# Optimization experiments

Hardware: AMD Instinct MI355X
Metric: run time of the kernel (lower is better)

Reference implementation:

```python
import jax, jax.numpy as jnp
import numpy as np

NUM_NODES = 512
INPUT_DIM = 64
HID_DIM = 64
K_DIFF = 2          # max_diffusion_step
N_LAYERS = 2
N_SUPPORTS = 1      # filter_type='laplacian'
NUM_MATS = N_SUPPORTS * K_DIFF + 1
CONCAT = INPUT_DIM + HID_DIM  # == HID_DIM + HID_DIM since input_dim == hid_dim


def setup_inputs() -> dict:
    key = jax.random.key(0)
    ks = jax.random.split(key, 8)
    T, B = 48, 32
    inputs = jax.random.normal(ks[0], (T, B, NUM_NODES * INPUT_DIM), dtype=jnp.float32)
    h0 = jnp.zeros((N_LAYERS, B, NUM_NODES * HID_DIM), dtype=jnp.float32)
    supports = jax.random.uniform(ks[1], (N_SUPPORTS, NUM_NODES, NUM_NODES), dtype=jnp.float32) / NUM_NODES
    s = 0.05
    W_gate = jax.random.normal(ks[2], (N_LAYERS, NUM_MATS * CONCAT, 2 * HID_DIM), dtype=jnp.float32) * s
    b_gate = jnp.ones((N_LAYERS, 2 * HID_DIM), dtype=jnp.float32)  # bias_start=1.0
    W_c = jax.random.normal(ks[3], (N_LAYERS, NUM_MATS * CONCAT, HID_DIM), dtype=jnp.float32) * s
    b_c = jnp.zeros((N_LAYERS, HID_DIM), dtype=jnp.float32)
    return {"inputs": inputs, "initial_hidden_state": h0, "supports": supports,
            "W_gate": W_gate, "b_gate": b_gate, "W_c": W_c, "b_c": b_c}


def _gconv(supports, x_flat, h_flat, W, b, out_dim):
    # x_flat: (B, N*d_in), h_flat: (B, N*hid)
    B = x_flat.shape[0]
    xh = jnp.concatenate([x_flat.reshape(B, NUM_NODES, -1),
                          h_flat.reshape(B, NUM_NODES, -1)], axis=-1)  # (B,N,c)
    mats = [xh]
    for i in range(N_SUPPORTS):
        S = supports[i]
        t0, t1 = xh, jnp.einsum('nm,bmc->bnc', S, xh)
        mats.append(t1)
        for _ in range(2, K_DIFF + 1):  # Chebyshev recurrence: x_k = 2 S x_{k-1} - x_{k-2}
            t2 = 2.0 * jnp.einsum('nm,bmc->bnc', S, t1) - t0
            mats.append(t2)
            t0, t1 = t1, t2
    feat = jnp.concatenate(mats, axis=-1)            # (B, N, NUM_MATS*c)
    out = jnp.einsum('bnf,fo->bno', feat, W) + b      # (B, N, out_dim)
    return out


def _dcgru_cell(supports, x, h, Wg, bg, Wc, bc):
    B = x.shape[0]
    gates = jax.nn.sigmoid(_gconv(supports, x, h, Wg, bg, 2 * HID_DIM))  # (B,N,2h)
    r, u = jnp.split(gates, 2, axis=-1)
    rh = (r * h.reshape(B, NUM_NODES, HID_DIM)).reshape(B, NUM_NODES * HID_DIM)
    c = jnp.tanh(_gconv(supports, x, rh, Wc, bc, HID_DIM))               # (B,N,h)
    h3 = h.reshape(B, NUM_NODES, HID_DIM)
    new_h = u * h3 + (1.0 - u) * c
    return new_h.reshape(B, NUM_NODES * HID_DIM)


def reference(inputs, initial_hidden_state, supports, W_gate, b_gate, W_c, b_c):
    current = inputs  # (T, B, N*d)
    final_hidden = []
    for l in range(N_LAYERS):
        def step(h, x, l=l):
            h2 = _dcgru_cell(supports, x, h, W_gate[l], b_gate[l], W_c[l], b_c[l])
            return h2, h2
        hT, outs = jax.lax.scan(step, initial_hidden_state[l], current)
        final_hidden.append(hT)
        current = outs
    return jnp.stack(final_hidden, axis=0), current
```

## Files before the change

kernel.cpp:

```cpp
#include <hip/hip_runtime.h>
#include <math.h>

typedef __bf16 bf16_t;
typedef bf16_t bf16x8 __attribute__((ext_vector_type(8)));
typedef bf16_t bf16x4 __attribute__((ext_vector_type(4)));
typedef float  f32x4  __attribute__((ext_vector_type(4)));
typedef unsigned long long u64_t;

#define NB 32
#define NN 512
#define NH 64
#define NF 384
#define TSTEPS 48

static __device__ __forceinline__ f32x4 mfma16(bf16x8 a, bf16x8 b, f32x4 c){
  return __builtin_amdgcn_mfma_f32_16x16x32_bf16(a, b, c, 0, 0, 0);
}
static __device__ __forceinline__ void gload16(char* lds, const char* g){
  __builtin_amdgcn_global_load_lds((const __attribute__((address_space(1))) void*)g,
                                   (__attribute__((address_space(3))) void*)lds, 16, 0, 0);
}
static __device__ __forceinline__ unsigned pack2(float a, float b){
  bf16_t x = (bf16_t)a, y = (bf16_t)b;
  unsigned short ux = __builtin_bit_cast(unsigned short, x);
  unsigned short uy = __builtin_bit_cast(unsigned short, y);
  return (unsigned)ux | ((unsigned)uy << 16);
}

__global__ __launch_bounds__(256) void k_s2f(const float* __restrict__ S,
                                             float* __restrict__ S2f){
  int idx = blockIdx.x * 256 + threadIdx.x;
  int n = idx >> 9, m = idx & 511;
  float acc = 0.f;
  #pragma unroll 8
  for (int k = 0; k < 512; ++k) acc += S[n * 512 + k] * S[k * 512 + m];
  S2f[idx] = acc;
}

__global__ __launch_bounds__(256) void k_prepS(const float* __restrict__ S,
                                               const float* __restrict__ S2f,
                                               char* __restrict__ dst){
  int id = blockIdx.x * 256 + threadIdx.x;
  int r = id >> 9, k = id & 511;
  float v = (r < 512) ? S[r * 512 + k] : S2f[(r - 512) * 512 + k];
  int rt = r >> 5, rr = r & 31, kt = k >> 6, kk = k & 63;
  size_t off = ((size_t)(rt * 8 + kt)) * 4096 + (size_t)(((rr * 128 + 2 * kk)) ^ ((rr & 7) << 4));
  *(bf16_t*)(dst + off) = (bf16_t)v;
}

__global__ __launch_bounds__(256) void k_prepW(const float* __restrict__ W,
                                               char* __restrict__ dst, int OD){
  int i = blockIdx.x * 256 + threadIdx.x;
  int total = 2 * NF * OD;
  if (i >= total) return;
  int l = i / (NF * OD), rem = i - l * (NF * OD);
  int o = rem / NF, f = rem - o * NF;
  const float* Wl = W + (size_t)l * NF * OD;
  float v;
  if (f < 128)      v = Wl[f * OD + o] - Wl[(256 + f) * OD + o];
  else if (f < 256) v = Wl[f * OD + o];
  else              v = 2.f * Wl[f * OD + o];
  int kt = f >> 6, kk = f & 63;
  size_t off = (size_t)l * (6 * OD * 128) + (size_t)kt * (OD * 128)
             + (size_t)(((o * 128 + 2 * kk)) ^ ((o & 7) << 4));
  *(bf16_t*)(dst + off) = (bf16_t)v;
}

__global__ __launch_bounds__(256) void k_hinit(const float* __restrict__ h0,
                                               float* __restrict__ hNf,
                                               bf16_t* __restrict__ hN){
  size_t i = ((size_t)blockIdx.x * 256 + threadIdx.x) * 8;
  f32x4 a = *(const f32x4*)&h0[i], b = *(const f32x4*)&h0[i + 4];
  *(f32x4*)&hNf[i] = a; *(f32x4*)&hNf[i + 4] = b;
  bf16x8 v;
  #pragma unroll
  for (int q = 0; q < 4; ++q){ v[q] = (bf16_t)a[q]; v[q + 4] = (bf16_t)b[q]; }
  *(bf16x8*)&hN[i] = v;
}

__global__ __launch_bounds__(512, 4) void k_gate(
    const float* __restrict__ inputs, const float* __restrict__ curp, int p,
    const bf16_t* __restrict__ hN, const char* __restrict__ SP,
    const char* __restrict__ WgP, const float* __restrict__ bga,
    bf16_t* __restrict__ rhN, float* __restrict__ uN, bf16_t* __restrict__ Dx)
{
  const int l = blockIdx.y;
  const int t = p - l;
  if (t < 0 || t >= TSTEPS) return;

  __shared__ char smem[81920];
  char* const A0 = smem;            char* const A1 = smem + 16384;
  char* const B0 = smem + 32768;    char* const B1 = smem + 49152;
  char* const FT = smem;
  char* const W0 = smem + 49152;
  char* const W1 = smem + 65536;
  char* const RL = smem + 49152;
  char* const UL = smem + 57344;

  const int L = blockIdx.x;
  const int b  = (L & 7) + ((L >> 6) << 3);
  const int bx = (L >> 3) & 7;
  const int n0 = bx * 64;
  const int tid = threadIdx.x, lane = tid & 63, w = tid >> 6;
  const int fr = lane & 15, ko = (lane >> 4) * 8, ro = (lane >> 4) * 4;
  const int pp = tid >> 4, q4 = tid & 15;
  const int wr = w >> 2, wc = w & 3;
  const int wn = w & 1, wo = w >> 1;

  const float* xall = l ? curp : inputs;
  const float*  xs = xall + ((size_t)t * NB + b) * NN * NH;
  const bf16_t* hbg = hN + ((size_t)(l * NB + b)) * NN * NH;
  const char* const WgPl = WgP + (size_t)l * 98304;
  const float* const bg = bga + l * 128;
  bf16_t* const rh_l = rhN + (size_t)l * NB * NN * NH;
  float*  const u_l  = uN  + (size_t)l * NB * NN * NH;
  bf16_t* const Dx_l = Dx  + (size_t)l * NB * NN * 128;

  f32x4 acc[4][2] = {};
  f32x4 rx0[2], rx1[2]; u64_t rh0[2], rh1[2];
  char* const Abuf[2] = { A0, A1 };
  char* const Bbuf[2] = { B0, B1 };

  auto ldB = [&](int kt, int s){
    int m = kt * 64 + 2 * pp;
    const float* xr = xs + (size_t)m * NH + q4 * 4;
    rx0[s] = *(const f32x4*)xr; rx1[s] = *(const f32x4*)(xr + NH);
    const bf16_t* hr = hbg + (size_t)m * NH + q4 * 4;
    rh0[s] = *(const u64_t*)hr; rh1[s] = *(const u64_t*)(hr + NH);
  };
  auto stB = [&](int s, char* Bb){
    int mby = 4 * pp;
    #pragma unroll
    for (int i = 0; i < 4; ++i){
      int c = q4 * 4 + i;
      *(unsigned*)(Bb + ((c * 128 + mby) ^ (((c >> 2) & 7) << 4))) = pack2(rx0[s][i], rx1[s][i]);
      int c2 = c + 64;
      unsigned uh = (unsigned)((rh0[s] >> (16 * i)) & 0xffffULL)
                  | ((unsigned)((rh1[s] >> (16 * i)) & 0xffffULL) << 16);
      *(unsigned*)(Bb + ((c2 * 128 + mby) ^ (((c2 >> 2) & 7) << 4))) = uh;
    }
  };
  auto gloadA = [&](int kt, char* Ab){
    #pragma unroll
    for (int i = 0; i < 2; ++i){
      int c = w * 2 + i;
      int ti = c >> 2;
      int rt = (ti < 2) ? (bx * 2 + ti) : (16 + bx * 2 + (ti - 2));
      gload16(Ab + c * 1024,
              SP + ((size_t)(rt * 8 + kt)) * 4096 + (c & 3) * 1024 + lane * 16);
    }
  };
  auto gloadW = [&](int j, char* Wb){
    const char* src = WgPl + (size_t)j * 16384 + (w * 64 + lane) * 16;
    gload16(Wb + w * 1024, src);
    gload16(Wb + 8192 + w * 1024, src + 8192);
  };
  auto dmm = [&](const char* Ab, const char* Bb){
    #pragma unroll
    for (int kh = 0; kh < 2; ++kh){
      int kb = 2 * (kh * 32 + ko);
      bf16x8 af[4], bf_[2];
      #pragma unroll
      for (int fm = 0; fm < 4; ++fm){
        int r = wr * 64 + fm * 16 + fr;
        af[fm] = *(const bf16x8*)(Ab + (r >> 5) * 4096 + ((((r & 31) * 128 + kb)) ^ ((r & 7) << 4)));
      }
      #pragma unroll
      for (int fc = 0; fc < 2; ++fc){
        int c = wc * 32 + fc * 16 + fr;
        bf_[fc] = *(const bf16x8*)(Bb + ((c * 128 + kb) ^ (((c >> 2) & 7) << 4)));
      }
      #pragma unroll
      for (int fm = 0; fm < 4; ++fm)
        #pragma unroll
        for (int fc = 0; fc < 2; ++fc)
          acc[fm][fc] = mfma16(af[fm], bf_[fc], acc[fm][fc]);
    }
  };

  gloadA(0, A0);
  ldB(0, 0); stB(0, B0);
  ldB(1, 1);
  __syncthreads();

  #pragma unroll
  for (int kt = 0; kt < 8; ++kt){
    if (kt < 7){
      gloadA(kt + 1, Abuf[(kt + 1) & 1]);
      stB((kt + 1) & 1, Bbuf[(kt + 1) & 1]);
    }
    dmm(Abuf[kt & 1], Bbuf[kt & 1]);
    __syncthreads();
    if (kt < 6) ldB(kt + 2, (kt + 2) & 1);
  }

  gloadW(0, W0); gloadW(1, W1);

  #pragma unroll
  for (int s = 0; s < 2; ++s){
    int i = tid + s * 512;
    int row = i >> 4, c8 = (i & 15) * 8;
    char* fdst = FT + (((row * 768 + 2 * c8)) ^ ((row & 7) << 4));
    if (c8 < 64){
      const float* xr = xs + (size_t)(n0 + row) * NH + c8;
      f32x4 a = *(const f32x4*)xr, bq = *(const f32x4*)(xr + 4);
      bf16x8 v;
      #pragma unroll
      for (int q = 0; q < 4; ++q){ v[q] = (bf16_t)a[q]; v[q + 4] = (bf16_t)bq[q]; }
      *(bf16x8*)fdst = v;
    } else {
      *(bf16x8*)fdst = *(const bf16x8*)(hbg + (size_t)(n0 + row) * NH + (c8 - 64));
    }
  }
  #pragma unroll
  for (int fm = 0; fm < 4; ++fm)
    #pragma unroll
    for (int fc = 0; fc < 2; ++fc)
      #pragma unroll
      for (int q = 0; q < 4; ++q){
        int dr = wr * 64 + fm * 16 + ro + q;
        int nn = dr & 63;
        int col = ((dr < 64) ? 128 : 256) + wc * 32 + fc * 16 + fr;
        *(bf16_t*)(FT + (((nn * 768 + 2 * col)) ^ ((nn & 7) << 4))) = (bf16_t)acc[fm][fc][q];
      }
  __syncthreads();

  #pragma unroll
  for (int s = 0; s < 2; ++s){
    int i = tid + s * 512;
    int row = i >> 4, d8 = (i & 15) * 8;
    int col = (d8 < 64) ? 128 + d8 : 256 + (d8 - 64);
    bf16x8 v = *(const bf16x8*)(FT + (((row * 768 + 2 * col)) ^ ((row & 7) << 4)));
    *(bf16x8*)&Dx_l[((size_t)b * NN + n0 + row) * 128 + d8] = v;
  }

  f32x4 gd[2][2] = {};
  #pragma unroll
  for (int j = 0; j < 6; ++j){
    const char* Wb = (j & 1) ? W1 : W0;
    #pragma unroll
    for (int kh = 0; kh < 2; ++kh){
      int kbf = 2 * (j * 64 + kh * 32 + ko);
      int kbw = 2 * (kh * 32 + ko);
      bf16x8 af[2];
      #pragma unroll
      for (int fm = 0; fm < 2; ++fm){
        int r = wn * 32 + fm * 16 + fr;
        af[fm] = *(const bf16x8*)(FT + ((r * 768 + kbf) ^ ((r & 7) << 4)));
      }
      #pragma unroll
      for (int fo = 0; fo < 2; ++fo){
        int orow = wo * 32 + fo * 16 + fr;
        bf16x8 bw = *(const bf16x8*)(Wb + ((orow * 128 + kbw) ^ ((orow & 7) << 4)));
        #pragma unroll
        for (int fm = 0; fm < 2; ++fm)
          gd[fm][fo] = mfma16(af[fm], bw, gd[fm][fo]);
      }
    }
    if (j != 4) __syncthreads();
    if (j < 4) gloadW(j + 2, (j & 1) ? W1 : W0);
  }

  #pragma unroll
  for (int fm = 0; fm < 2; ++fm)
    #pragma unroll
    for (int fo = 0; fo < 2; ++fo){
      int o = wo * 32 + fo * 16 + fr;
      float bias = bg[o];
      #pragma unroll
      for (int q = 0; q < 4; ++q){
        int nn = wn * 32 + fm * 16 + ro + q;
        float g = 1.f / (1.f + __expf(-(gd[fm][fo][q] + bias)));
        if (o < 64){
          float hv = (float)*(const bf16_t*)(FT + (((nn * 768 + 2 * (64 + o))) ^ ((nn & 7) << 4)));
          *(bf16_t*)(RL + ((nn * 128 + 2 * o) ^ ((nn & 7) << 4))) = (bf16_t)(g * hv);
        } else {
          *(float*)(UL + ((nn * 256 + 4 * (o - 64)) ^ ((nn & 7) << 5))) = g;
        }
      }
    }
  __syncthreads();
  {
    int row = tid >> 3, o8 = (tid & 7) * 8;
    bf16x8 v = *(const bf16x8*)(RL + ((row * 128 + 2 * o8) ^ ((row & 7) << 4)));
    *(bf16x8*)&rh_l[((size_t)b * NN + n0 + row) * NH + o8] = v;
    int base = (row * 256 + 4 * o8) ^ ((row & 7) << 5);
    f32x4 u0 = *(const f32x4*)(UL + base);
    f32x4 u1 = *(const f32x4*)(UL + base + 16);
    size_t gi = ((size_t)b * NN + n0 + row) * NH + o8;
    *(f32x4*)&u_l[gi] = u0; *(f32x4*)&u_l[gi + 4] = u1;
  }
}

__global__ __launch_bounds__(512, 4) void k_cand(
    const float* __restrict__ inputs, int p,
    const bf16_t* __restrict__ rhN, const bf16_t* __restrict__ Dx,
    const char* __restrict__ SP, const char* __restrict__ WcP,
    const float* __restrict__ bca, const float* __restrict__ uN,
    float* __restrict__ hNf, bf16_t* __restrict__ hN,
    float* __restrict__ outp)
{
  const int l = blockIdx.y;
  const int t = p - l;
  if (t < 0 || t >= TSTEPS) return;

  __shared__ char smem[81920];
  char* const A0 = smem;            char* const A1 = smem + 16384;
  char* const B0 = smem + 32768;    char* const B1 = smem + 40960;
  char* const FT = smem;
  char* const W0 = smem + 49152;    char* const W1 = smem + 65536;
  char* const CL = smem + 49152;

  const int L = blockIdx.x;
  const int b  = (L & 7) + ((L >> 6) << 3);
  const int bx = (L >> 3) & 7;
  const int n0 = bx * 64;
  const int tid = threadIdx.x, lane = tid & 63, w = tid >> 6;
  const int fr = lane & 15, ko = (lane >> 4) * 8, ro = (lane >> 4) * 4;
  const int pp = tid >> 4, q4 = tid & 15;
  const int wr = w >> 2, wc = w & 3;
  const int wn = w & 1, wo = w >> 1;

  float* const cur = outp + (size_t)2 * NB * NN * NH;
  const float* xall = l ? cur : inputs;
  const float*  xs = xall + ((size_t)t * NB + b) * NN * NH;
  const bf16_t* rbg = rhN + ((size_t)(l * NB + b)) * NN * NH;
  const char* const WcPl = WcP + (size_t)l * 49152;
  const float* const bc = bca + l * 64;
  const bf16_t* const Dx_l = Dx + (size_t)l * NB * NN * 128;
  const float* const u_l = uN + (size_t)l * NB * NN * NH;
  float*  const hNf_l = hNf + (size_t)l * NB * NN * NH;
  bf16_t* const hN_l  = hN  + (size_t)l * NB * NN * NH;
  float* const fin = outp + (size_t)l * NB * NN * NH;

  f32x4 ca[4] = {};
  u64_t rh0[2], rh1[2];
  char* const Abuf[2] = { A0, A1 };
  char* const Bbuf[2] = { B0, B1 };

  auto ldB = [&](int kt, int s){
    int m = kt * 64 + 2 * pp;
    const bf16_t* rr = rbg + (size_t)m * NH + q4 * 4;
    rh0[s] = *(const u64_t*)rr; rh1[s] = *(const u64_t*)(rr + NH);
  };
  auto stB = [&](int s, char* Bb){
    int mby = 4 * pp;
    #pragma unroll
    for (int i = 0; i < 4; ++i){
      int c = q4 * 4 + i;
      unsigned u = (unsigned)((rh0[s] >> (16 * i)) & 0xffffULL)
                 | ((unsigned)((rh1[s] >> (16 * i)) & 0xffffULL) << 16);
      *(unsigned*)(Bb + ((c * 128 + mby) ^ (((c >> 2) & 7) << 4))) = u;
    }
  };
  auto gloadA = [&](int kt, char* Ab){
    #pragma unroll
    for (int i = 0; i < 2; ++i){
      int c = w * 2 + i;
      int ti = c >> 2;
      int rt = (ti < 2) ? (bx * 2 + ti) : (16 + bx * 2 + (ti - 2));
      gload16(Ab + c * 1024,
              SP + ((size_t)(rt * 8 + kt)) * 4096 + (c & 3) * 1024 + lane * 16);
    }
  };
  auto gloadW2 = [&](int j, char* Wb){
    const char* src = WcPl + (size_t)(2 * j) * 8192 + (w * 64 + lane) * 16;
    gload16(Wb + w * 1024, src);
    gload16(Wb + 8192 + w * 1024, src + 8192);
  };
  auto cmm = [&](const char* Ab, const char* Bb){
    #pragma unroll
    for (int kh = 0; kh < 2; ++kh){
      int kb = 2 * (kh * 32 + ko);
      int c = wc * 16 + fr;
      bf16x8 bf_ = *(const bf16x8*)(Bb + ((c * 128 + kb) ^ (((c >> 2) & 7) << 4)));
      #pragma unroll
      for (int fm = 0; fm < 4; ++fm){
        int r = wr * 64 + fm * 16 + fr;
        bf16x8 af = *(const bf16x8*)(Ab + (r >> 5) * 4096 + ((((r & 31) * 128 + kb)) ^ ((r & 7) << 4)));
        ca[fm] = mfma16(af, bf_, ca[fm]);
      }
    }
  };

  gloadA(0, A0);
  gloadW2(0, W0); gloadW2(1, W1);
  ldB(0, 0); stB(0, B0);
  ldB(1, 1);
  __syncthreads();

  #pragma unroll
  for (int kt = 0; kt < 8; ++kt){
    if (kt < 7){
      gloadA(kt + 1, Abuf[(kt + 1) & 1]);
      stB((kt + 1) & 1, Bbuf[(kt + 1) & 1]);
    }
    cmm(Abuf[kt & 1], Bbuf[kt & 1]);
    __syncthreads();
    if (kt < 6) ldB(kt + 2, (kt + 2) & 1);
  }

  #pragma unroll
  for (int s = 0; s < 2; ++s){
    int i = tid + s * 512;
    int row = i >> 4, c8 = (i & 15) * 8;
    char* fdst = FT + (((row * 768 + 2 * c8)) ^ ((row & 7) << 4));
    if (c8 < 64){
      const float* xr = xs + (size_t)(n0 + row) * NH + c8;
      f32x4 a = *(const f32x4*)xr, bq = *(const f32x4*)(xr + 4);
      bf16x8 v;
      #pragma unroll
      for (int q = 0; q < 4; ++q){ v[q] = (bf16_t)a[q]; v[q + 4] = (bf16_t)bq[q]; }
      *(bf16x8*)fdst = v;
    } else {
      *(bf16x8*)fdst = *(const bf16x8*)(rbg + (size_t)(n0 + row) * NH + (c8 - 64));
    }
    int col = (c8 < 64) ? 128 + c8 : 256 + (c8 - 64);
    bf16x8 dv = *(const bf16x8*)&Dx_l[((size_t)b * NN + n0 + row) * 128 + c8];
    *(bf16x8*)(FT + (((row * 768 + 2 * col)) ^ ((row & 7) << 4))) = dv;
  }
  #pragma unroll
  for (int fm = 0; fm < 4; ++fm)
    #pragma unroll
    for (int q = 0; q < 4; ++q){
      int dr = wr * 64 + fm * 16 + ro + q;
      int nn = dr & 63;
      int col = ((dr < 64) ? 192 : 320) + wc * 16 + fr;
      *(bf16_t*)(FT + (((nn * 768 + 2 * col)) ^ ((nn & 7) << 4))) = (bf16_t)ca[fm][q];
    }
  __syncthreads();

  f32x4 cd[2] = {};
  #pragma unroll
  for (int j = 0; j < 3; ++j){
    const char* Wb = (j & 1) ? W1 : W0;
    #pragma unroll
    for (int kh = 0; kh < 4; ++kh){
      int kbf = 2 * (j * 128 + kh * 32 + ko);
      int sub = (kh >= 2) ? 8192 : 0;
      int kbw = 2 * ((kh & 1) * 32 + ko);
      int orow = wo * 16 + fr;
      bf16x8 bw = *(const bf16x8*)(Wb + sub + ((orow * 128 + kbw) ^ ((orow & 7) << 4)));
      #pragma unroll
      for (int fm = 0; fm < 2; ++fm){
        int r = wn * 32 + fm * 16 + fr;
        bf16x8 af = *(const bf16x8*)(FT + ((r * 768 + kbf) ^ ((r & 7) << 4)));
        cd[fm] = mfma16(af, bw, cd[fm]);
      }
    }
    __syncthreads();
    if (j == 0) gloadW2(2, W0);
  }

  #pragma unroll
  for (int fm = 0; fm < 2; ++fm){
    int o = wo * 16 + fr;
    float bias = bc[o];
    #pragma unroll
    for (int q = 0; q < 4; ++q){
      int nn = wn * 32 + fm * 16 + ro + q;
      float e = __expf(2.f * (cd[fm][q] + bias));
      *(float*)(CL + ((nn * 256 + 4 * o) ^ ((nn & 7) << 5))) = (e - 1.f) / (e + 1.f);
    }
  }
  __syncthreads();
  {
    int row = tid >> 3, o8 = (tid & 7) * 8;
    int base = (row * 256 + 4 * o8) ^ ((row & 7) << 5);
    f32x4 c0 = *(const f32x4*)(CL + base);
    f32x4 c1 = *(const f32x4*)(CL + base + 16);
    size_t gi = ((size_t)b * NN + n0 + row) * NH + o8;
    f32x4 u0 = *(const f32x4*)&u_l[gi], u1 = *(const f32x4*)&u_l[gi + 4];
    f32x4 h0v = *(const f32x4*)&hNf_l[gi], h1v = *(const f32x4*)&hNf_l[gi + 4];
    f32x4 n0v, n1v;
    #pragma unroll
    for (int q = 0; q < 4; ++q){
      n0v[q] = u0[q] * h0v[q] + (1.f - u0[q]) * c0[q];
      n1v[q] = u1[q] * h1v[q] + (1.f - u1[q]) * c1[q];
    }
    *(f32x4*)&hNf_l[gi] = n0v; *(f32x4*)&hNf_l[gi + 4] = n1v;
    bf16x8 hb;
    #pragma unroll
    for (int q = 0; q < 4; ++q){ hb[q] = (bf16_t)n0v[q]; hb[q + 4] = (bf16_t)n1v[q]; }
    *(bf16x8*)&hN_l[gi] = hb;
    float* cr = cur + (size_t)t * NB * NN * NH + gi;
    *(f32x4*)cr = n0v; *(f32x4*)(cr + 4) = n1v;
    if (t == TSTEPS - 1){
      *(f32x4*)&fin[gi] = n0v; *(f32x4*)&fin[gi + 4] = n1v;
    }
  }
}

extern "C" void kernel_launch(void* const* d_in, const int* in_sizes, int n_in,
                              void* d_out, int out_size, void* d_ws, size_t ws_size,
                              hipStream_t stream){
  const float* inputs = (const float*)d_in[0];
  const float* h0     = (const float*)d_in[1];
  const float* S      = (const float*)d_in[2];
  const float* W_gate = (const float*)d_in[3];
  const float* b_gate = (const float*)d_in[4];
  const float* W_c    = (const float*)d_in[5];
  const float* b_c    = (const float*)d_in[6];
  float* out = (float*)d_out;
  char* ws = (char*)d_ws;

  char*   SP  =          ws + 0;
  char*   WgP =          ws + 1048576;
  char*   WcP =          ws + 1245184;
  float*  hNf = (float*) (ws + 1343488);
  bf16_t* hN  = (bf16_t*)(ws + 9732096);
  bf16_t* rhN = (bf16_t*)(ws + 13926400);
  float*  uN  = (float*) (ws + 18120704);
  bf16_t* Dx  = (bf16_t*)(ws + 26509312);
  float*  S2f = (float*) (ws + 26509312 + 4194304);

  k_s2f<<<dim3(1024), 256, 0, stream>>>(S, S2f);
  k_prepS<<<dim3(2048), 256, 0, stream>>>(S, S2f, SP);
  k_prepW<<<dim3(384), 256, 0, stream>>>(W_gate, WgP, 128);
  k_prepW<<<dim3(192), 256, 0, stream>>>(W_c, WcP, 64);
  k_hinit<<<dim3(1024), 256, 0, stream>>>(h0, hNf, hN);

  for (int p = 0; p <= TSTEPS; ++p){
    k_gate<<<dim3(256, 2), 512, 0, stream>>>(inputs, out + (size_t)2 * NB * NN * NH,
                                             p, hN, SP, WgP, b_gate, rhN, uN, Dx);
    k_cand<<<dim3(256, 2), 512, 0, stream>>>(inputs, p, rhN, Dx, SP, WcP, b_c, uN,
                                             hNf, hN, out);
  }
}
```

Before: 2.183 ms.

## Fuse gate and candidate kernels with per-batch inter-block barrier

Merges the gate and candidate graph-convolution kernels into a single per-timestep kernel. The 8 blocks that share a batch index synchronise through an atomic counter/generation barrier in workspace, instead of relying on a kernel boundary. This halves the number of launches in the time loop and removes the full-grid drain between the two phases. In exchange it relies on all 8 blocks of a group being co-resident. The spin loop has an iteration cap that silently breaks out, which could produce wrong results if the blocks are not scheduled together.

```diff
diff --git a/kernel.cpp b/kernel.cpp
--- a/kernel.cpp
+++ b/kernel.cpp
@@ -78,17 +78,33 @@
   *(bf16x8*)&hN[i] = v;
 }
 
-__global__ __launch_bounds__(512, 4) void k_gate(
-    const float* __restrict__ inputs, const float* __restrict__ curp, int p,
+__device__ __forceinline__ void gbarrier8(unsigned* cnt, unsigned* gen){
+  __syncthreads();
+  if (threadIdx.x == 0){
+    __threadfence();
+    unsigned gc = __hip_atomic_load(gen, __ATOMIC_RELAXED, __HIP_MEMORY_SCOPE_AGENT);
+    unsigned a  = __hip_atomic_fetch_add(cnt, 1u, __ATOMIC_ACQ_REL, __HIP_MEMORY_SCOPE_AGENT);
+    if (a == 7u){
+      __hip_atomic_store(cnt, 0u, __ATOMIC_RELAXED, __HIP_MEMORY_SCOPE_AGENT);
+      __hip_atomic_fetch_add(gen, 1u, __ATOMIC_RELEASE, __HIP_MEMORY_SCOPE_AGENT);
+    } else {
+      long sp = 0;
+      while (__hip_atomic_load(gen, __ATOMIC_ACQUIRE, __HIP_MEMORY_SCOPE_AGENT) == gc){
+        __builtin_amdgcn_s_sleep(1);
+        if (++sp > (1L << 22)) break;
+      }
+    }
+    __threadfence();
+  }
+  __syncthreads();
+}
+
+__device__ __forceinline__ void gate_body(char* smem, int l, int t,
+    const float* __restrict__ inputs, const float* __restrict__ curp,
     const bf16_t* __restrict__ hN, const char* __restrict__ SP,
     const char* __restrict__ WgP, const float* __restrict__ bga,
     bf16_t* __restrict__ rhN, float* __restrict__ uN, bf16_t* __restrict__ Dx)
 {
-  const int l = blockIdx.y;
-  const int t = p - l;
-  if (t < 0 || t >= TSTEPS) return;
-
-  __shared__ char smem[81920];
   char* const A0 = smem;            char* const A1 = smem + 16384;
   char* const B0 = smem + 32768;    char* const B1 = smem + 49152;
   char* const FT = smem;
@@ -292,19 +308,14 @@
   }
 }
 
-__global__ __launch_bounds__(512, 4) void k_cand(
-    const float* __restrict__ inputs, int p,
+__device__ __forceinline__ void cand_body(char* smem, int l, int t,
+    const float* __restrict__ inputs,
     const bf16_t* __restrict__ rhN, const bf16_t* __restrict__ Dx,
     const char* __restrict__ SP, const char* __restrict__ WcP,
     const float* __restrict__ bca, const float* __restrict__ uN,
     float* __restrict__ hNf, bf16_t* __restrict__ hN,
     float* __restrict__ outp)
 {
-  const int l = blockIdx.y;
-  const int t = p - l;
-  if (t < 0 || t >= TSTEPS) return;
-
-  __shared__ char smem[81920];
   char* const A0 = smem;            char* const A1 = smem + 16384;
   char* const B0 = smem + 32768;    char* const B1 = smem + 40960;
   char* const FT = smem;
@@ -489,6 +500,30 @@
       *(f32x4*)&fin[gi] = n0v; *(f32x4*)&fin[gi + 4] = n1v;
     }
   }
+}
+
+__global__ __launch_bounds__(512, 4) void k_step(int p,
+    const float* __restrict__ inputs, const char* __restrict__ SP,
+    const char* __restrict__ WgP, const char* __restrict__ WcP,
+    const float* __restrict__ bga, const float* __restrict__ bca,
+    bf16_t* __restrict__ rhN, float* __restrict__ uN, bf16_t* __restrict__ Dx,
+    float* __restrict__ hNf, bf16_t* __restrict__ hN,
+    unsigned* __restrict__ bar, float* __restrict__ outp)
+{
+  __shared__ char smem[81920];
+  const int l = blockIdx.y;
+  const int t = p - l;
+  if (t < 0 || t >= TSTEPS) return;
+
+  const int L = blockIdx.x;
+  const int b = (L & 7) + ((L >> 6) << 3);
+  unsigned* const bcnt = bar + (l * 32 + b) * 32;
+  unsigned* const bgen = bcnt + 1;
+
+  gate_body(smem, l, t, inputs, outp + (size_t)2 * NB * NN * NH,
+            hN, SP, WgP, bga, rhN, uN, Dx);
+  gbarrier8(bcnt, bgen);
+  cand_body(smem, l, t, inputs, rhN, Dx, SP, WcP, bca, uN, hNf, hN, outp);
 }
 
 extern "C" void kernel_launch(void* const* d_in, const int* in_sizes, int n_in,
@@ -504,16 +539,18 @@
   float* out = (float*)d_out;
   char* ws = (char*)d_ws;
 
-  char*   SP  =          ws + 0;
-  char*   WgP =          ws + 1048576;
-  char*   WcP =          ws + 1245184;
-  float*  hNf = (float*) (ws + 1343488);
-  bf16_t* hN  = (bf16_t*)(ws + 9732096);
-  bf16_t* rhN = (bf16_t*)(ws + 13926400);
-  float*  uN  = (float*) (ws + 18120704);
-  bf16_t* Dx  = (bf16_t*)(ws + 26509312);
-  float*  S2f = (float*) (ws + 26509312 + 4194304);
-
+  char*    SP  =           ws + 0;
+  char*    WgP =           ws + 1048576;
+  char*    WcP =           ws + 1245184;
+  float*   hNf = (float*)  (ws + 1343488);
+  bf16_t*  hN  = (bf16_t*) (ws + 9732096);
+  bf16_t*  rhN = (bf16_t*) (ws + 13926400);
+  float*   uN  = (float*)  (ws + 18120704);
+  bf16_t*  Dx  = (bf16_t*) (ws + 26509312);
+  unsigned* bar = (unsigned*)(ws + 34897920);
+  float*   S2f = (float*)  (ws + 26509312 + 4194304);
+
+  hipMemsetAsync(bar, 0, 8192, stream);
   k_s2f<<<dim3(1024), 256, 0, stream>>>(S, S2f);
   k_prepS<<<dim3(2048), 256, 0, stream>>>(S, S2f, SP);
   k_prepW<<<dim3(384), 256, 0, stream>>>(W_gate, WgP, 128);
@@ -521,9 +558,8 @@
   k_hinit<<<dim3(1024), 256, 0, stream>>>(h0, hNf, hN);
 
   for (int p = 0; p <= TSTEPS; ++p){
-    k_gate<<<dim3(256, 2), 512, 0, stream>>>(inputs, out + (size_t)2 * NB * NN * NH,
-                                             p, hN, SP, WgP, b_gate, rhN, uN, Dx);
-    k_cand<<<dim3(256, 2), 512, 0, stream>>>(inputs, p, rhN, Dx, SP, WcP, b_c, uN,
-                                             hNf, hN, out);
-  }
-}
+    k_step<<<dim3(256, 2), 512, 0, stream>>>(p, inputs, SP, WgP, WcP,
+                                             b_gate, b_c, rhN, uN, Dx,
+                                             hNf, hN, bar, out);
+  }
+}
```

New measurement: 6.161 ms. +182.2%, slower.
